# Kernel optimization log

Measured on AMD Instinct MI355X. Metric: run time of the kernel, lower is better.

The kernel has to match this reference:

```python
import jax, jax.numpy as jnp
import numpy as np

N, E, G = 50000, 800000, 64
IN_C, HID, HEADS, OUT_C = 128, 64, 4, 10
NEG_SLOPE = 0.2
EPS = 1e-16


def gat_conv(x, src, dst, W, a_src, a_dst, bias, heads, out_ch):
    # x: [N, F_in]; W: [F_in, heads*out_ch]; a_*: [heads, out_ch]; bias: [heads*out_ch]
    n = x.shape[0]
    h = (x @ W).reshape(n, heads, out_ch)                     # [N, H, C]
    alpha_src = jnp.einsum('nhc,hc->nh', h, a_src)            # [N, H]
    alpha_dst = jnp.einsum('nhc,hc->nh', h, a_dst)            # [N, H]
    e = jax.nn.leaky_relu(alpha_src[src] + alpha_dst[dst], NEG_SLOPE)  # [E, H]
    # segment softmax over incoming edges of each destination node
    m = jax.ops.segment_max(e, dst, num_segments=n)
    ex = jnp.exp(e - m[dst])
    denom = jax.ops.segment_sum(ex, dst, num_segments=n)
    alpha = ex / (denom[dst] + EPS)                           # [E, H]
    msg = h[src] * alpha[:, :, None]                          # [E, H, C]
    out = jax.ops.segment_sum(msg, dst, num_segments=n)       # [N, H, C]
    return out.reshape(n, heads * out_ch) + bias


def setup_inputs() -> dict:
    key = jax.random.key(0)
    ks = jax.random.split(key, 16)
    s = 0.1
    inp = {
        'x': jax.random.normal(ks[0], (N, IN_C), dtype=jnp.float32),
        'edge_index': jax.random.randint(ks[1], (2, E), 0, N, dtype=jnp.int64)
            if jax.config.jax_enable_x64 else jax.random.randint(ks[1], (2, E), 0, N).astype(jnp.int32),
        'batch': jnp.sort(jax.random.randint(ks[2], (N,), 0, G).astype(jnp.int32)),
        'W1': s * jax.random.normal(ks[3], (IN_C, HEADS * HID), dtype=jnp.float32),
        'as1': s * jax.random.normal(ks[4], (HEADS, HID), dtype=jnp.float32),
        'ad1': s * jax.random.normal(ks[5], (HEADS, HID), dtype=jnp.float32),
        'b1': jnp.zeros((HEADS * HID,), jnp.float32),
        'W2': s * jax.random.normal(ks[6], (HEADS * HID, HEADS * HID), dtype=jnp.float32),
        'as2': s * jax.random.normal(ks[7], (HEADS, HID), dtype=jnp.float32),
        'ad2': s * jax.random.normal(ks[8], (HEADS, HID), dtype=jnp.float32),
        'b2': jnp.zeros((HEADS * HID,), jnp.float32),
        'W3': s * jax.random.normal(ks[9], (HEADS * HID, HID), dtype=jnp.float32),
        'as3': s * jax.random.normal(ks[10], (1, HID), dtype=jnp.float32),
        'ad3': s * jax.random.normal(ks[11], (1, HID), dtype=jnp.float32),
        'b3': jnp.zeros((HID,), jnp.float32),
        'Wc': s * jax.random.normal(ks[12], (HID, OUT_C), dtype=jnp.float32),
        'bc': jnp.zeros((OUT_C,), jnp.float32),
    }
    return inp


def reference(x, edge_index, batch, W1, as1, ad1, b1, W2, as2, ad2, b2,
              W3, as3, ad3, b3, Wc, bc):
    n = x.shape[0]
    loop = jnp.arange(n, dtype=edge_index.dtype)
    src = jnp.concatenate([edge_index[0], loop])  # add self-loops (PyG default)
    dst = jnp.concatenate([edge_index[1], loop])

    h = gat_conv(x, src, dst, W1, as1, ad1, b1, HEADS, HID)
    h = jax.nn.elu(h)
    h = gat_conv(h, src, dst, W2, as2, ad2, b2, HEADS, HID)
    h = jax.nn.elu(h)
    h = gat_conv(h, src, dst, W3, as3, ad3, b3, 1, HID)

    # global mean pool over graphs
    sums = jax.ops.segment_sum(h, batch, num_segments=G)            # [G, HID]
    counts = jax.ops.segment_sum(jnp.ones((n,), h.dtype), batch, num_segments=G)
    pooled = sums / jnp.maximum(counts, 1.0)[:, None]

    logits = pooled @ Wc + bc                                       # [G, OUT_C]
    return logits
```

## Files before the change

kernel.cpp:

```cpp
#include <hip/hip_runtime.h>

#define NEG_SLOPE 0.2f
#define EPSV 1e-16f

typedef unsigned short ushort_t;
typedef unsigned char uchar_t;
typedef __attribute__((ext_vector_type(8))) short bf16x8;
typedef __attribute__((ext_vector_type(4))) float f32x4;
typedef __attribute__((ext_vector_type(2))) float f32x2;

__device__ __forceinline__ ushort_t f2bf(float f) {
    union { float f; unsigned u; } v; v.f = f;
    unsigned r = v.u + 0x7FFFu + ((v.u >> 16) & 1u);
    return (ushort_t)(r >> 16);
}
__device__ __forceinline__ float bf2f(ushort_t u) {
    union { unsigned u; float f; } v; v.u = ((unsigned)u) << 16;
    return v.f;
}
__device__ __forceinline__ uchar_t f2fp8(float f) {
    int p = __builtin_amdgcn_cvt_pk_fp8_f32(f, 0.f, 0, false);
    return (uchar_t)(p & 0xff);
}

__global__ __launch_bounds__(256)
void count_kernel(const int* __restrict__ ei, int* __restrict__ deg8, int E, int n) {
    int i = blockIdx.x * blockDim.x + threadIdx.x;
    int M = E + n;
    if (i >= M) return;
    int d = (i < E) ? ei[E + i] : (i - E);
    atomicAdd(&deg8[(blockIdx.x & 7) * n + d], 1);
}

__global__ __launch_bounds__(1024)
void scan1_kernel(const int* __restrict__ deg8, int* __restrict__ indptr,
                  int* __restrict__ bsum, int n) {
    __shared__ int wsum[16];
    const int t = threadIdx.x;
    const int lane = t & 63;
    const int w = t >> 6;
    const int i = blockIdx.x * 1024 + t;
    int v = 0;
    if (i < n) {
        #pragma unroll
        for (int j = 0; j < 8; ++j) v += deg8[j * n + i];
    }
    int s = v;
    #pragma unroll
    for (int off = 1; off < 64; off <<= 1) {
        int u = __shfl_up(s, off);
        if (lane >= off) s += u;
    }
    if (lane == 63) wsum[w] = s;
    __syncthreads();
    if (t < 16) {
        int ws_ = wsum[t];
        #pragma unroll
        for (int off = 1; off < 16; off <<= 1) {
            int u = __shfl_up(ws_, off);
            if (t >= off) ws_ += u;
        }
        wsum[t] = ws_;
    }
    __syncthreads();
    int woff = (w > 0) ? wsum[w - 1] : 0;
    if (i < n) indptr[i + 1] = woff + s;
    if (t == 0) bsum[blockIdx.x] = wsum[15];
}

__global__ __launch_bounds__(1024)
void scan3_kernel(int* __restrict__ indptr, int* __restrict__ deg8,
                  const int* __restrict__ bsum, int nb, int n) {
    __shared__ int boff_s;
    const int t = threadIdx.x;
    const int i = blockIdx.x * 1024 + t;
    int lv1 = (i < n) ? indptr[i + 1] : 0;
    int lv0 = (i < n && t > 0) ? indptr[i] : 0;
    if (t < 64) {
        int v = (t < nb) ? bsum[t] : 0;
        int s = v;
        #pragma unroll
        for (int off = 1; off < 64; off <<= 1) {
            int u = __shfl_up(s, off);
            if (t >= off) s += u;
        }
        if (t == (int)blockIdx.x) boff_s = s - v;
    }
    __syncthreads();
    const int boff = boff_s;
    if (i < n) {
        indptr[i + 1] = lv1 + boff;
        int running = (t == 0) ? boff : lv0 + boff;
        #pragma unroll
        for (int j = 0; j < 8; ++j) {
            int c = deg8[j * n + i];
            deg8[j * n + i] = running;
            running += c;
        }
    }
    if (i == 0) indptr[0] = 0;
}

__global__ __launch_bounds__(256)
void scatter_kernel(const int* __restrict__ ei, int* __restrict__ cursor8,
                    unsigned* __restrict__ csrp, int E, int n) {
    int i = blockIdx.x * blockDim.x + threadIdx.x;
    int M = E + n;
    if (i >= M) return;
    int s, d;
    if (i < E) { s = ei[i]; d = ei[E + i]; }
    else       { s = i - E; d = i - E; }
    int pos = atomicAdd(&cursor8[(blockIdx.x & 7) * n + d], 1);
    csrp[pos] = (unsigned)s | ((unsigned)d << 16);
}

__global__ __launch_bounds__(256)
void prep_kernel(const float* __restrict__ x, ushort_t* __restrict__ xb, int nx4,
                 const float* __restrict__ W1, ushort_t* __restrict__ Wt1,
                 const float* __restrict__ W2, ushort_t* __restrict__ Wt2,
                 const float* __restrict__ W3, ushort_t* __restrict__ Wt3,
                 int K1, int* __restrict__ deg8, int n8,
                 int* __restrict__ poolz, int gz) {
    long idx = (long)blockIdx.x * 256 + threadIdx.x;
    if (idx < nx4) {
        float4 v = *reinterpret_cast<const float4*>(&x[idx * 4]);
        ushort4 o;
        o.x = f2bf(v.x); o.y = f2bf(v.y); o.z = f2bf(v.z); o.w = f2bf(v.w);
        *reinterpret_cast<ushort4*>(&xb[idx * 4]) = o;
        return;
    }
    idx -= nx4;
    if (idx < (long)K1 * 256) {
        int c = (int)(idx % 256), k = (int)(idx / 256);
        Wt1[(long)c * K1 + k] = f2bf(W1[idx]);
        return;
    }
    idx -= (long)K1 * 256;
    if (idx < 256 * 256) {
        int c = (int)(idx % 256), k = (int)(idx / 256);
        Wt2[(long)c * 256 + k] = f2bf(W2[idx]);
        return;
    }
    idx -= 256 * 256;
    if (idx < 256 * 64) {
        int c = (int)(idx % 64), k = (int)(idx / 64);
        Wt3[(long)c * 256 + k] = f2bf(W3[idx]);
        return;
    }
    idx -= 256 * 64;
    if (idx < n8) { deg8[idx] = 0; return; }
    idx -= n8;
    if (idx < gz) poolz[idx] = 0;
}

template<int NC>
__global__ __launch_bounds__(256)
void mfma_gemm_alpha_kernel(const ushort_t* __restrict__ A, const ushort_t* __restrict__ Wt,
                            uchar_t* __restrict__ C,
                            const float* __restrict__ a_src, const float* __restrict__ a_dst,
                            float* __restrict__ asrc, float* __restrict__ adst,
                            int M, int K, int N, int H) {
    constexpr int TBN = NC * 64;
    constexpr int MI  = (NC == 2) ? 4 : 2;
    __shared__ ushort_t As[128][40];
    __shared__ ushort_t Ws[TBN][40];
    const int tid  = threadIdx.x;
    const int w    = tid >> 6;
    const int lane = tid & 63;
    const int l15  = lane & 15;
    const int l4   = lane >> 4;
    const int row0 = blockIdx.x * 128;
    const int col0 = blockIdx.y * TBN;
    const int rbase = (NC == 2) ? (w & 1) * 64 : w * 32;
    const int cbase = (NC == 2) ? (w >> 1) * 64 : 0;

    f32x4 acc[MI][4];
    #pragma unroll
    for (int mi = 0; mi < MI; ++mi)
        #pragma unroll
        for (int ni = 0; ni < 4; ++ni)
            acc[mi][ni] = (f32x4){0.f, 0.f, 0.f, 0.f};

    for (int k0 = 0; k0 < K; k0 += 32) {
        #pragma unroll
        for (int it = 0; it < 2; ++it) {
            int idx = tid + it * 256;
            int r = idx >> 2, seg = idx & 3;
            int gr = row0 + r;
            uint4 v = make_uint4(0u, 0u, 0u, 0u);
            if (gr < M)
                v = *reinterpret_cast<const uint4*>(&A[(long)gr * K + k0 + seg * 8]);
            *reinterpret_cast<uint4*>(&As[r][seg * 8]) = v;
        }
        #pragma unroll
        for (int it = 0; it < NC; ++it) {
            int idx = tid + it * 256;
            int r = idx >> 2, seg = idx & 3;
            uint4 v = *reinterpret_cast<const uint4*>(&Wt[(long)(col0 + r) * K + k0 + seg * 8]);
            *reinterpret_cast<uint4*>(&Ws[r][seg * 8]) = v;
        }
        __syncthreads();
        bf16x8 af[MI], bfv[4];
        #pragma unroll
        for (int mi = 0; mi < MI; ++mi)
            af[mi] = *reinterpret_cast<const bf16x8*>(&As[rbase + mi * 16 + l15][8 * l4]);
        #pragma unroll
        for (int ni = 0; ni < 4; ++ni)
            bfv[ni] = *reinterpret_cast<const bf16x8*>(&Ws[cbase + ni * 16 + l15][8 * l4]);
        #pragma unroll
        for (int mi = 0; mi < MI; ++mi)
            #pragma unroll
            for (int ni = 0; ni < 4; ++ni)
                acc[mi][ni] = __builtin_amdgcn_mfma_f32_16x16x32_bf16(
                    af[mi], bfv[ni], acc[mi][ni], 0, 0, 0);
        __syncthreads();
    }

    #pragma unroll
    for (int mi = 0; mi < MI; ++mi)
        #pragma unroll
        for (int reg = 0; reg < 4; ++reg) {
            int gr = row0 + rbase + mi * 16 + l4 * 4 + reg;
            if (gr < M) {
                #pragma unroll
                for (int ni = 0; ni < 4; ++ni)
                    C[(long)gr * N + col0 + cbase + ni * 16 + l15] = f2fp8(acc[mi][ni][reg]);
            }
        }

    const int hd = (col0 + cbase) >> 6;
    float aS[4], aD[4];
    #pragma unroll
    for (int ni = 0; ni < 4; ++ni) {
        aS[ni] = a_src[hd * 64 + ni * 16 + l15];
        aD[ni] = a_dst[hd * 64 + ni * 16 + l15];
    }
    #pragma unroll
    for (int mi = 0; mi < MI; ++mi)
        #pragma unroll
        for (int reg = 0; reg < 4; ++reg) {
            float s = 0.f, d = 0.f;
            #pragma unroll
            for (int ni = 0; ni < 4; ++ni) {
                s += acc[mi][ni][reg] * aS[ni];
                d += acc[mi][ni][reg] * aD[ni];
            }
            #pragma unroll
            for (int off = 1; off < 16; off <<= 1) {
                s += __shfl_xor(s, off);
                d += __shfl_xor(d, off);
            }
            int gr = row0 + rbase + mi * 16 + l4 * 4 + reg;
            if (l15 == 0 && gr < M) {
                asrc[gr * H + hd] = s;
                adst[gr * H + hd] = d;
            }
        }
}

__global__ __launch_bounds__(256)
void edgeexp4_kernel(const unsigned* __restrict__ csrp,
                     const float4* __restrict__ asrc4, const float4* __restrict__ adst4,
                     float4* __restrict__ ex4, int M) {
    int i = blockIdx.x * blockDim.x + threadIdx.x;
    if (i >= M) return;
    unsigned v = csrp[i];
    int s = (int)(v & 0xffffu), d = (int)(v >> 16);
    float4 a = asrc4[s];
    float4 b = adst4[d];
    float e, ex_, ey_, ez_, ew_;
    e = a.x + b.x; e = e > 0.f ? e : NEG_SLOPE * e; ex_ = __expf(e);
    e = a.y + b.y; e = e > 0.f ? e : NEG_SLOPE * e; ey_ = __expf(e);
    e = a.z + b.z; e = e > 0.f ? e : NEG_SLOPE * e; ez_ = __expf(e);
    e = a.w + b.w; e = e > 0.f ? e : NEG_SLOPE * e; ew_ = __expf(e);
    ex4[i] = make_float4(ex_, ey_, ez_, ew_);
}

__global__ __launch_bounds__(256)
void edgeexp1_kernel(const unsigned* __restrict__ csrp,
                     const float* __restrict__ asrc, const float* __restrict__ adst,
                     float* __restrict__ ex1, int M) {
    int i = blockIdx.x * blockDim.x + threadIdx.x;
    if (i >= M) return;
    unsigned v = csrp[i];
    float e = asrc[v & 0xffffu] + adst[v >> 16];
    e = e > 0.f ? e : NEG_SLOPE * e;
    ex1[i] = __expf(e);
}

__global__ __launch_bounds__(256)
void aggregate4_kernel(const uchar_t* __restrict__ h, const float* __restrict__ ex4,
                       const int* __restrict__ indptr, const unsigned* __restrict__ csrp,
                       const float* __restrict__ bias, ushort_t* __restrict__ out,
                       int n, int apply_elu) {
    const int node = (blockIdx.x * blockDim.x + threadIdx.x) >> 6;
    const int lane = threadIdx.x & 63;
    if (node >= n) return;
    const int hd  = lane >> 4;
    const int beg = indptr[node], end = indptr[node + 1];
    const int cnt = end - beg;
    const uchar_t* __restrict__ hrow = h + 4 * lane;
    const float* __restrict__ exh = ex4 + 4 * (long)beg + hd;

    float sum_ex = 0.f;
    float ax = 0.f, ay = 0.f, az = 0.f, aw = 0.f;
    int i = 0;
    for (; i + 8 <= cnt; i += 8) {
        long s[8];
        float ee[8];
        unsigned v[8];
        #pragma unroll
        for (int u = 0; u < 8; ++u) s[u] = (long)(csrp[beg + i + u] & 0xffffu);
        #pragma unroll
        for (int u = 0; u < 8; ++u) ee[u] = exh[(long)(i + u) * 4];
        #pragma unroll
        for (int u = 0; u < 8; ++u)
            v[u] = *reinterpret_cast<const unsigned*>(hrow + (s[u] << 8));
        #pragma unroll
        for (int u = 0; u < 8; ++u) {
            f32x2 lo = __builtin_amdgcn_cvt_pk_f32_fp8((int)v[u], false);
            f32x2 hi = __builtin_amdgcn_cvt_pk_f32_fp8((int)v[u], true);
            sum_ex += ee[u];
            ax += ee[u] * lo[0];
            ay += ee[u] * lo[1];
            az += ee[u] * hi[0];
            aw += ee[u] * hi[1];
        }
    }
    for (; i < cnt; ++i) {
        long s = (long)(csrp[beg + i] & 0xffffu);
        float ee = exh[(long)i * 4];
        unsigned v = *reinterpret_cast<const unsigned*>(hrow + (s << 8));
        f32x2 lo = __builtin_amdgcn_cvt_pk_f32_fp8((int)v, false);
        f32x2 hi = __builtin_amdgcn_cvt_pk_f32_fp8((int)v, true);
        sum_ex += ee;
        ax += ee * lo[0]; ay += ee * lo[1];
        az += ee * hi[0]; aw += ee * hi[1];
    }
    const float inv = 1.f / (sum_ex + EPSV);
    float4 b4 = *reinterpret_cast<const float4*>(bias + 4 * lane);
    float ox = ax * inv + b4.x;
    float oy = ay * inv + b4.y;
    float oz = az * inv + b4.z;
    float ow = aw * inv + b4.w;
    if (apply_elu) {
        ox = ox > 0.f ? ox : expm1f(ox);
        oy = oy > 0.f ? oy : expm1f(oy);
        oz = oz > 0.f ? oz : expm1f(oz);
        ow = ow > 0.f ? ow : expm1f(ow);
    }
    ushort4 o4;
    o4.x = f2bf(ox); o4.y = f2bf(oy); o4.z = f2bf(oz); o4.w = f2bf(ow);
    *reinterpret_cast<ushort4*>(out + (long)node * 256 + 4 * lane) = o4;
}

__global__ __launch_bounds__(256)
void aggregate_kernel(const uchar_t* __restrict__ h, const float* __restrict__ ex1,
                      const int* __restrict__ indptr, const unsigned* __restrict__ csrp,
                      const float* __restrict__ bias, ushort_t* __restrict__ out,
                      int n, int apply_elu) {
    const int node = (blockIdx.x * blockDim.x + threadIdx.x) >> 6;
    const int lane = threadIdx.x & 63;
    if (node >= n) return;
    const int beg = indptr[node], end = indptr[node + 1];
    const int cnt = end - beg;
    const uchar_t* __restrict__ hh = h + lane;

    float sum_ex = 0.f, acc = 0.f;
    int i = 0;
    for (; i + 8 <= cnt; i += 8) {
        long s[8];
        float ee[8];
        uchar_t b[8];
        #pragma unroll
        for (int u = 0; u < 8; ++u) s[u] = (long)(csrp[beg + i + u] & 0xffffu);
        #pragma unroll
        for (int u = 0; u < 8; ++u) ee[u] = ex1[beg + i + u];
        #pragma unroll
        for (int u = 0; u < 8; ++u) b[u] = hh[s[u] << 6];
        #pragma unroll
        for (int u = 0; u < 8; ++u) {
            f32x2 r = __builtin_amdgcn_cvt_pk_f32_fp8((int)b[u], false);
            sum_ex += ee[u];
            acc += ee[u] * r[0];
        }
    }
    for (; i < cnt; ++i) {
        long s = (long)(csrp[beg + i] & 0xffffu);
        float ee = ex1[beg + i];
        f32x2 r = __builtin_amdgcn_cvt_pk_f32_fp8((int)hh[s << 6], false);
        sum_ex += ee;
        acc += ee * r[0];
    }
    float o = acc / (sum_ex + EPSV) + bias[lane];
    if (apply_elu) o = o > 0.f ? o : expm1f(o);
    out[(long)node * 64 + lane] = f2bf(o);
}

constexpr int POOL_CHUNK = 128;

__global__ __launch_bounds__(64)
void pool_kernel(const ushort_t* __restrict__ h, const int* __restrict__ batch,
                 float* __restrict__ sums, int* __restrict__ counts, int n) {
    int lane = threadIdx.x;
    int start = blockIdx.x * POOL_CHUNK;
    if (start >= n) return;
    int end = min(start + POOL_CHUNK, n);
    int gcur = batch[start];
    float acc = 0.f;
    int run = 0;
    for (int i = start; i < end; ++i) {
        int g = batch[i];
        if (g != gcur) {
            atomicAdd(&sums[gcur * 64 + lane], acc);
            if (lane == 0) atomicAdd(&counts[gcur], run);
            acc = 0.f; run = 0; gcur = g;
        }
        acc += bf2f(h[(long)i * 64 + lane]);
        ++run;
    }
    atomicAdd(&sums[gcur * 64 + lane], acc);
    if (lane == 0) atomicAdd(&counts[gcur], run);
}

__global__ void classify_kernel(const float* __restrict__ sums, const int* __restrict__ counts,
                                const float* __restrict__ Wc, const float* __restrict__ bc,
                                float* __restrict__ out, int G) {
    int t = threadIdx.x;
    if (t >= G * 10) return;
    int g = t / 10, o = t - g * 10;
    int c_ = counts[g];
    float inv = 1.f / (float)(c_ > 1 ? c_ : 1);
    float acc = bc[o];
    for (int c = 0; c < 64; ++c)
        acc += sums[g * 64 + c] * inv * Wc[c * 10 + o];
    out[t] = acc;
}

extern "C" void kernel_launch(void* const* d_in, const int* in_sizes, int n_in,
                              void* d_out, int out_size, void* d_ws, size_t ws_size,
                              hipStream_t stream) {
    const float* x   = (const float*)d_in[0];
    const int*   ei  = (const int*)d_in[1];
    const int*   bat = (const int*)d_in[2];
    const float* W1  = (const float*)d_in[3];
    const float* as1 = (const float*)d_in[4];
    const float* ad1 = (const float*)d_in[5];
    const float* b1  = (const float*)d_in[6];
    const float* W2  = (const float*)d_in[7];
    const float* as2 = (const float*)d_in[8];
    const float* ad2 = (const float*)d_in[9];
    const float* b2  = (const float*)d_in[10];
    const float* W3  = (const float*)d_in[11];
    const float* as3 = (const float*)d_in[12];
    const float* ad3 = (const float*)d_in[13];
    const float* b3  = (const float*)d_in[14];
    const float* Wc  = (const float*)d_in[15];
    const float* bc  = (const float*)d_in[16];
    float* out = (float*)d_out;

    const int N = in_sizes[2];
    const int E = in_sizes[1] / 2;
    const int M = E + N;
    const int IN_C = in_sizes[0] / N;
    const int G = out_size / 10;

    char* p = (char*)d_ws;
    auto carve = [&](size_t bytes) -> void* {
        void* r = (void*)p;
        p += (bytes + 255) & ~(size_t)255;
        return r;
    };
    uchar_t*  hA  = (uchar_t*)carve((size_t)N * 256);
    ushort_t* hB  = (ushort_t*)carve((size_t)N * 256 * 2);
    size_t xb_ex_bytes = (size_t)M * 16;
    size_t xb_need = (size_t)N * IN_C * 2;
    if (xb_need > xb_ex_bytes) xb_ex_bytes = xb_need;
    ushort_t* xb  = (ushort_t*)carve(xb_ex_bytes);
    float*    ex  = (float*)xb;
    ushort_t* Wt1 = (ushort_t*)carve((size_t)256 * IN_C * 2);
    ushort_t* Wt2 = (ushort_t*)carve((size_t)256 * 256 * 2);
    ushort_t* Wt3 = (ushort_t*)carve((size_t)64 * 256 * 2);
    float* asrc = (float*)carve((size_t)N * 4 * 4);
    float* adst = (float*)carve((size_t)N * 4 * 4);
    float* sums = (float*)carve((size_t)G * 64 * 4 + (size_t)G * 4);
    int*   cnts = (int*)(sums + (size_t)G * 64);
    int*   deg8 = (int*)carve((size_t)8 * N * 4);
    int*   iptr = (int*)carve((size_t)(N + 1) * 4);
    unsigned* csrp = (unsigned*)carve((size_t)M * 4);
    int*   bsum = (int*)carve(256 * 4);
    (void)ws_size; (void)n_in;

    const int NB = (N + 1023) / 1024;
    const int MB = (M + 255) / 256;
    const int AGB = (N + 3) / 4;

    {
        long nx4 = (long)N * IN_C / 4;
        int gz = G * 65;
        long total = nx4 + (long)IN_C * 256 + 256 * 256 + 256 * 64 + 8L * N + gz;
        prep_kernel<<<(int)((total + 255) / 256), 256, 0, stream>>>(
            x, xb, (int)nx4, W1, Wt1, W2, Wt2, W3, Wt3, IN_C, deg8, 8 * N, (int*)sums, gz);
    }

    count_kernel<<<MB, 256, 0, stream>>>(ei, deg8, E, N);
    scan1_kernel<<<NB, 1024, 0, stream>>>(deg8, iptr, bsum, N);
    scan3_kernel<<<NB, 1024, 0, stream>>>(iptr, deg8, bsum, NB, N);
    scatter_kernel<<<MB, 256, 0, stream>>>(ei, deg8, csrp, E, N);

    {
        dim3 grid((N + 127) / 128, 2);
        mfma_gemm_alpha_kernel<2><<<grid, 256, 0, stream>>>(xb, Wt1, hA, as1, ad1,
                                                            asrc, adst, N, IN_C, 256, 4);
    }
    edgeexp4_kernel<<<MB, 256, 0, stream>>>(csrp, (const float4*)asrc,
                                            (const float4*)adst, (float4*)ex, M);
    aggregate4_kernel<<<AGB, 256, 0, stream>>>(hA, ex, iptr, csrp, b1, hB, N, 1);

    {
        dim3 grid((N + 127) / 128, 2);
        mfma_gemm_alpha_kernel<2><<<grid, 256, 0, stream>>>(hB, Wt2, hA, as2, ad2,
                                                            asrc, adst, N, 256, 256, 4);
    }
    edgeexp4_kernel<<<MB, 256, 0, stream>>>(csrp, (const float4*)asrc,
                                            (const float4*)adst, (float4*)ex, M);
    aggregate4_kernel<<<AGB, 256, 0, stream>>>(hA, ex, iptr, csrp, b2, hB, N, 1);

    {
        dim3 grid((N + 127) / 128, 1);
        mfma_gemm_alpha_kernel<1><<<grid, 256, 0, stream>>>(hB, Wt3, hA, as3, ad3,
                                                            asrc, adst, N, 256, 64, 1);
    }
    edgeexp1_kernel<<<MB, 256, 0, stream>>>(csrp, asrc, adst, ex, M);
    aggregate_kernel<<<AGB, 256, 0, stream>>>(hA, ex, iptr, csrp, b3, hB, N, 0);

    pool_kernel<<<(N + POOL_CHUNK - 1) / POOL_CHUNK, 64, 0, stream>>>(hB, bat, sums, cnts, N);
    classify_kernel<<<1, 640, 0, stream>>>(sums, cnts, Wc, bc, out, G);
}
```

Measured before the change: 448.1 us.

## Build CSR via two-level bucket sort with shared-memory atomics

Replaces the global-atomic count/scatter CSR construction, which used 8-way replicated per-node counters, with a two-pass bucket sort. Edges are first binned into 256-node buckets using block-local histograms and one global atomic per bucket. Per-bucket kernels then count degrees and scatter into CSR positions using shared-memory atomics. This cuts global atomic contention and random writes, but adds a fixed-capacity bucket buffer (BCAP=6144) that would overflow if a bucket receives too many edges.

New measurement: 393.4 us. 1.14x faster.

```diff
diff --git a/kernel.cpp b/kernel.cpp
--- a/kernel.cpp
+++ b/kernel.cpp
@@ -2,6 +2,7 @@
 
 #define NEG_SLOPE 0.2f
 #define EPSV 1e-16f
+#define BCAP 6144
 
 typedef unsigned short ushort_t;
 typedef unsigned char uchar_t;
@@ -24,27 +25,66 @@
 }
 
 __global__ __launch_bounds__(256)
-void count_kernel(const int* __restrict__ ei, int* __restrict__ deg8, int E, int n) {
-    int i = blockIdx.x * blockDim.x + threadIdx.x;
-    int M = E + n;
-    if (i >= M) return;
-    int d = (i < E) ? ei[E + i] : (i - E);
-    atomicAdd(&deg8[(blockIdx.x & 7) * n + d], 1);
+void bucketA_kernel(const int* __restrict__ ei, int* __restrict__ gcursor,
+                    unsigned* __restrict__ bbuf, int E, int n, int nbuk) {
+    __shared__ int hist[256];
+    __shared__ int base[256];
+    const int t = threadIdx.x;
+    const long cb = (long)blockIdx.x * 4096;
+    const int M = E + n;
+    hist[t] = 0;
+    __syncthreads();
+    unsigned entry[16];
+    int bk[16], lr[16];
+    #pragma unroll
+    for (int j = 0; j < 16; ++j) {
+        long i = cb + j * 256 + t;
+        bk[j] = -1;
+        if (i < M) {
+            int s, d;
+            if (i < E) { s = ei[i]; d = ei[E + i]; }
+            else       { s = (int)(i - E); d = s; }
+            int b = d >> 8;
+            bk[j] = b;
+            entry[j] = (unsigned)s | ((unsigned)(d & 255) << 16);
+            lr[j] = atomicAdd(&hist[b], 1);
+        }
+    }
+    __syncthreads();
+    if (t < nbuk && hist[t] > 0) base[t] = atomicAdd(&gcursor[t], hist[t]);
+    __syncthreads();
+    #pragma unroll
+    for (int j = 0; j < 16; ++j)
+        if (bk[j] >= 0)
+            bbuf[(long)bk[j] * BCAP + base[bk[j]] + lr[j]] = entry[j];
+}
+
+__global__ __launch_bounds__(256)
+void bucketB1_kernel(const unsigned* __restrict__ bbuf, const int* __restrict__ gcursor,
+                     int* __restrict__ deg, int n) {
+    __shared__ int cnt[256];
+    const int t = threadIdx.x;
+    const int b = blockIdx.x;
+    cnt[t] = 0;
+    __syncthreads();
+    const int nb = gcursor[b];
+    const unsigned* bp = bbuf + (long)b * BCAP;
+    for (int e = t; e < nb; e += 256)
+        atomicAdd(&cnt[(bp[e] >> 16) & 255], 1);
+    __syncthreads();
+    int d = (b << 8) + t;
+    if (d < n) deg[d] = cnt[t];
 }
 
 __global__ __launch_bounds__(1024)
-void scan1_kernel(const int* __restrict__ deg8, int* __restrict__ indptr,
+void scan1_kernel(const int* __restrict__ deg, int* __restrict__ indptr,
                   int* __restrict__ bsum, int n) {
     __shared__ int wsum[16];
     const int t = threadIdx.x;
     const int lane = t & 63;
     const int w = t >> 6;
     const int i = blockIdx.x * 1024 + t;
-    int v = 0;
-    if (i < n) {
-        #pragma unroll
-        for (int j = 0; j < 8; ++j) v += deg8[j * n + i];
-    }
+    int v = (i < n) ? deg[i] : 0;
     int s = v;
     #pragma unroll
     for (int off = 1; off < 64; off <<= 1) {
@@ -69,13 +109,10 @@
 }
 
 __global__ __launch_bounds__(1024)
-void scan3_kernel(int* __restrict__ indptr, int* __restrict__ deg8,
-                  const int* __restrict__ bsum, int nb, int n) {
+void scan3_kernel(int* __restrict__ indptr, const int* __restrict__ bsum,
+                  int nb, int n) {
     __shared__ int boff_s;
     const int t = threadIdx.x;
-    const int i = blockIdx.x * 1024 + t;
-    int lv1 = (i < n) ? indptr[i + 1] : 0;
-    int lv0 = (i < n && t > 0) ? indptr[i] : 0;
     if (t < 64) {
         int v = (t < nb) ? bsum[t] : 0;
         int s = v;
@@ -88,30 +125,28 @@
     }
     __syncthreads();
     const int boff = boff_s;
-    if (i < n) {
-        indptr[i + 1] = lv1 + boff;
-        int running = (t == 0) ? boff : lv0 + boff;
-        #pragma unroll
-        for (int j = 0; j < 8; ++j) {
-            int c = deg8[j * n + i];
-            deg8[j * n + i] = running;
-            running += c;
-        }
-    }
+    int i = blockIdx.x * 1024 + t;
+    if (i < n) indptr[i + 1] += boff;
     if (i == 0) indptr[0] = 0;
 }
 
 __global__ __launch_bounds__(256)
-void scatter_kernel(const int* __restrict__ ei, int* __restrict__ cursor8,
-                    unsigned* __restrict__ csrp, int E, int n) {
-    int i = blockIdx.x * blockDim.x + threadIdx.x;
-    int M = E + n;
-    if (i >= M) return;
-    int s, d;
-    if (i < E) { s = ei[i]; d = ei[E + i]; }
-    else       { s = i - E; d = i - E; }
-    int pos = atomicAdd(&cursor8[(blockIdx.x & 7) * n + d], 1);
-    csrp[pos] = (unsigned)s | ((unsigned)d << 16);
+void bucketB2_kernel(const unsigned* __restrict__ bbuf, const int* __restrict__ gcursor,
+                     const int* __restrict__ indptr, unsigned* __restrict__ csrp, int n) {
+    __shared__ int cur[256];
+    const int t = threadIdx.x;
+    const int b = blockIdx.x;
+    int d = (b << 8) + t;
+    cur[t] = (d < n) ? indptr[d] : 0;
+    __syncthreads();
+    const int nb = gcursor[b];
+    const unsigned* bp = bbuf + (long)b * BCAP;
+    for (int e = t; e < nb; e += 256) {
+        unsigned v = bp[e];
+        int d8 = (v >> 16) & 255;
+        int pos = atomicAdd(&cur[d8], 1);
+        csrp[pos] = (v & 0xffffu) | ((unsigned)((b << 8) + d8) << 16);
+    }
 }
 
 __global__ __launch_bounds__(256)
@@ -119,7 +154,7 @@
                  const float* __restrict__ W1, ushort_t* __restrict__ Wt1,
                  const float* __restrict__ W2, ushort_t* __restrict__ Wt2,
                  const float* __restrict__ W3, ushort_t* __restrict__ Wt3,
-                 int K1, int* __restrict__ deg8, int n8,
+                 int K1, int* __restrict__ gcursor, int nbuk,
                  int* __restrict__ poolz, int gz) {
     long idx = (long)blockIdx.x * 256 + threadIdx.x;
     if (idx < nx4) {
@@ -148,8 +183,8 @@
         return;
     }
     idx -= 256 * 64;
-    if (idx < n8) { deg8[idx] = 0; return; }
-    idx -= n8;
+    if (idx < nbuk) { gcursor[idx] = 0; return; }
+    idx -= nbuk;
     if (idx < gz) poolz[idx] = 0;
 }
 
@@ -464,6 +499,7 @@
     const int M = E + N;
     const int IN_C = in_sizes[0] / N;
     const int G = out_size / 10;
+    const int NBUK = (N + 255) >> 8;
 
     char* p = (char*)d_ws;
     auto carve = [&](size_t bytes) -> void* {
@@ -485,7 +521,9 @@
     float* adst = (float*)carve((size_t)N * 4 * 4);
     float* sums = (float*)carve((size_t)G * 64 * 4 + (size_t)G * 4);
     int*   cnts = (int*)(sums + (size_t)G * 64);
-    int*   deg8 = (int*)carve((size_t)8 * N * 4);
+    unsigned* bbuf = (unsigned*)carve((size_t)NBUK * BCAP * 4);
+    int*   gcursor = (int*)carve((size_t)NBUK * 4);
+    int*   deg  = (int*)carve((size_t)N * 4);
     int*   iptr = (int*)carve((size_t)(N + 1) * 4);
     unsigned* csrp = (unsigned*)carve((size_t)M * 4);
     int*   bsum = (int*)carve(256 * 4);
@@ -498,15 +536,16 @@
     {
         long nx4 = (long)N * IN_C / 4;
         int gz = G * 65;
-        long total = nx4 + (long)IN_C * 256 + 256 * 256 + 256 * 64 + 8L * N + gz;
+        long total = nx4 + (long)IN_C * 256 + 256 * 256 + 256 * 64 + NBUK + gz;
         prep_kernel<<<(int)((total + 255) / 256), 256, 0, stream>>>(
-            x, xb, (int)nx4, W1, Wt1, W2, Wt2, W3, Wt3, IN_C, deg8, 8 * N, (int*)sums, gz);
-    }
-
-    count_kernel<<<MB, 256, 0, stream>>>(ei, deg8, E, N);
-    scan1_kernel<<<NB, 1024, 0, stream>>>(deg8, iptr, bsum, N);
-    scan3_kernel<<<NB, 1024, 0, stream>>>(iptr, deg8, bsum, NB, N);
-    scatter_kernel<<<MB, 256, 0, stream>>>(ei, deg8, csrp, E, N);
+            x, xb, (int)nx4, W1, Wt1, W2, Wt2, W3, Wt3, IN_C, gcursor, NBUK, (int*)sums, gz);
+    }
+
+    bucketA_kernel<<<(M + 4095) / 4096, 256, 0, stream>>>(ei, gcursor, bbuf, E, N, NBUK);
+    bucketB1_kernel<<<NBUK, 256, 0, stream>>>(bbuf, gcursor, deg, N);
+    scan1_kernel<<<NB, 1024, 0, stream>>>(deg, iptr, bsum, N);
+    scan3_kernel<<<NB, 1024, 0, stream>>>(iptr, bsum, NB, N);
+    bucketB2_kernel<<<NBUK, 256, 0, stream>>>(bbuf, gcursor, iptr, csrp, N);
 
     {
         dim3 grid((N + 127) / 128, 2);
```
